# Optimization experiments

Measured on AMD Instinct MI355X. Metric: run time of the kernel, lower is better.

The kernel has to match this reference:

```python
import jax, jax.numpy as jnp
import numpy as np

DIMS = [3, 64, 64, 64, 3]  # [input_dim] + hidden dims + [input_dim]
TOTAL_W = sum(DIMS[l] * DIMS[l + 1] + 4 * DIMS[l + 1] for l in range(len(DIMS) - 1))  # 9356


def setup_inputs() -> dict:
    key = jax.random.key(0)
    k1, k2, k3 = jax.random.split(key, 3)
    B, N = 64, 8192
    context = jax.random.normal(k1, (B, N), dtype=jnp.float32)
    y = jax.random.normal(k2, (B, N, DIMS[0]), dtype=jnp.float32)
    tnw = jax.random.normal(k3, (B, TOTAL_W), dtype=jnp.float32) * 0.1
    return {"context": context, "y": y, "target_networks_weights": tnw}


def reference(context, y, target_networks_weights):
    B = target_networks_weights.shape[0]
    dx = y  # [B, N, dims[0]]
    i = 0
    n_layers = len(DIMS) - 1
    for l in range(n_layers):
        dl, dl1 = DIMS[l], DIMS[l + 1]
        W = target_networks_weights[:, i:i + dl * dl1].reshape(B, dl, dl1)
        i += dl * dl1
        bias = target_networks_weights[:, i:i + dl1]          # [B, dl1]
        i += dl1
        w_scale = target_networks_weights[:, i:i + dl1]        # [B, dl1]
        i += dl1
        b_scale = target_networks_weights[:, i:i + dl1]        # [B, dl1]
        i += dl1
        w_shift = target_networks_weights[:, i:i + dl1]        # [B, dl1]
        i += dl1
        # batched matmul + bias
        dx = jnp.einsum('bnd,bde->bne', dx, W) + bias[:, None, :]
        # sigmoid gate: bmm(context[:, :, None], w_scale[:, None, :]) = outer product
        scale = jax.nn.sigmoid(context[:, :, None] * w_scale[:, None, :] + b_scale[:, None, :])
        dx = scale * dx
        # shift term
        dx = dx + context[:, :, None] * w_shift[:, None, :]
        if l < n_layers - 1:
            dx = jax.nn.softplus(dx)
    return dx
```

## Files before the change

kernel.cpp:

```cpp
#include <hip/hip_runtime.h>
#include <math.h>

#define BB 64
#define NN 8192
#define TOTAL_W 9356

typedef _Float16 f16x8 __attribute__((ext_vector_type(8)));
typedef float f32x4 __attribute__((ext_vector_type(4)));
typedef float f32x2 __attribute__((ext_vector_type(2)));
typedef unsigned int u32x2 __attribute__((ext_vector_type(2)));

#define L2E 1.44269504088896340736f
#define LN2 0.6931471805599453f

#define FILM2_OFF 0
#define A1_OFF    4096
#define A2_OFF    (A1_OFF + 8192)
#define ACT_OFF   (A2_OFF + 8192)
#define LDS_BYTES (ACT_OFF + 128 * 128)

#define MFMA16(a, b, c) __builtin_amdgcn_mfma_f32_16x16x32_f16(a, b, c, 0, 0, 0)
#define EXP2 __builtin_amdgcn_exp2f
#define LOG2 __builtin_amdgcn_logf
#define RCPF __builtin_amdgcn_rcpf

__device__ __forceinline__ f32x2 pfma(f32x2 a, f32x2 b, f32x2 c) {
  return __builtin_elementwise_fma(a, b, c);
}

__device__ __forceinline__ const f32x4* film_base(const unsigned char* smem, int l, int qd) {
  return (const f32x4*)(smem + FILM2_OFF + ((l * 16 + qd) << 6));
}

template<bool SP>
__device__ __forceinline__ u32x2 film_quad(f32x4 acc, float ctx,
                                           f32x4 wscq, f32x4 bscq, f32x4 wshq) {
  f32x2 ctx2 = {ctx, ctx};
  f32x2 one = {1.f, 1.f};
  f32x2 z0 = pfma(ctx2, (f32x2){wscq.x, wscq.y}, (f32x2){bscq.x, bscq.y});
  f32x2 z1 = pfma(ctx2, (f32x2){wscq.z, wscq.w}, (f32x2){bscq.z, bscq.w});
  f32x2 d0 = {EXP2(-z0.x), EXP2(-z0.y)};  d0 += one;
  f32x2 d1 = {EXP2(-z1.x), EXP2(-z1.y)};  d1 += one;
  f32x2 s0 = {RCPF(d0.x), RCPF(d0.y)};
  f32x2 s1 = {RCPF(d1.x), RCPF(d1.y)};
  f32x2 v0 = pfma(ctx2, (f32x2){wshq.x, wshq.y}, s0 * (f32x2){acc.x, acc.y});
  f32x2 v1 = pfma(ctx2, (f32x2){wshq.z, wshq.w}, s1 * (f32x2){acc.z, acc.w});
  if (SP) {
    f32x2 l2 = {L2E, L2E}, ln = {LN2, LN2};
    f32x2 t0 = v0 * l2, t1 = v1 * l2;
    f32x2 u0 = {EXP2(t0.x), EXP2(t0.y)};  u0 += one;
    f32x2 u1 = {EXP2(t1.x), EXP2(t1.y)};  u1 += one;
    f32x2 g0 = {LOG2(u0.x), LOG2(u0.y)};
    f32x2 g1 = {LOG2(u1.x), LOG2(u1.y)};
    v0 = g0 * ln;
    v1 = g1 * ln;
  }
  auto p01 = __builtin_amdgcn_cvt_pkrtz(v0.x, v0.y);
  auto p23 = __builtin_amdgcn_cvt_pkrtz(v1.x, v1.y);
  u32x2 w;
  w.x = __builtin_bit_cast(unsigned int, p01);
  w.y = __builtin_bit_cast(unsigned int, p23);
  return w;
}

__device__ __forceinline__ void act_store(unsigned char* smem, int pt, int slot, u32x2 w) {
  int pos = ((((slot >> 1) ^ (pt & 7)) << 1) | (slot & 1));
  *(u32x2*)(smem + ACT_OFF + pt * 128 + (pos << 3)) = w;
}
__device__ __forceinline__ f16x8 act_load(const unsigned char* smem, int pt, int pair) {
  int gr = pair ^ (pt & 7);
  return *(const f16x8*)(smem + ACT_OFF + pt * 128 + (gr << 4));
}

__global__ __launch_bounds__(256)
void ode_hypernet_kernel(const float* __restrict__ context,
                         const float* __restrict__ y,
                         const float* __restrict__ tnw,
                         float* __restrict__ out) {
  __shared__ __align__(16) unsigned char smem[LDS_BYTES];
  const int b = blockIdx.y;
  const int tid = threadIdx.x;
  const float* __restrict__ wb = tnw + (size_t)b * TOTAL_W;

  const int lane = tid & 63;
  const int wid = tid >> 6;
  const int g = lane >> 4;
  const int col = lane & 15;

  if (tid < 64) {
    const int biaso[4] = {192, 4544, 8896, 9344};
    const int dim[4] = {64, 64, 64, 3};
#pragma unroll
    for (int l = 0; l < 4; ++l) {
      float bv = 0.f, wscv = 0.f, bscv = 0.f, wshv = 0.f;
      if (tid < dim[l]) {
        int bo = biaso[l], d = dim[l];
        bv = wb[bo + tid];
        wscv = wb[bo + d + tid] * L2E;
        bscv = wb[bo + 2 * d + tid] * L2E;
        wshv = wb[bo + 3 * d + tid];
      }
      float* f2 = (float*)(smem + FILM2_OFF + ((l * 16 + (tid >> 2)) << 6)) + (tid & 3);
      f2[0] = bv;
      f2[4] = wscv;
      f2[8] = bscv;
      f2[12] = wshv;
    }
  }
#pragma unroll
  for (int L = 0; L < 2; ++L) {
    const int woff = L ? 4800 : 448;
    const int aoff = L ? A2_OFF : A1_OFF;
#pragma unroll
    for (int it = 0; it < 4; ++it) {
      int idx = tid + it * 256;
      int f_in = idx >> 4;
      int q = idx & 15;
      f32x4 w4 = *(const f32x4*)(wb + woff + f_in * 64 + q * 4);
      int m = q >> 2;
      int c4 = (q & 3) * 4;
      int t = f_in >> 5;
      int h = (f_in >> 3) & 3;
      int i = f_in & 7;
      unsigned char* base = smem + aoff + (m * 128 + t * 64 + h * 16 + c4) * 16 + i * 2;
#pragma unroll
      for (int j = 0; j < 4; ++j)
        *(_Float16*)(base + j * 16) = (_Float16)w4[j];
    }
  }
  f16x8 A0r[4];
#pragma unroll
  for (int m = 0; m < 4; ++m) {
#pragma unroll
    for (int i = 0; i < 8; ++i)
      A0r[m][i] = (g == 0 && i < 3) ? (_Float16)wb[i * 64 + 16 * m + col] : (_Float16)0.f;
  }
  f16x8 A3r0, A3r1;
#pragma unroll
  for (int i = 0; i < 8; ++i) {
    A3r0[i] = (col < 3) ? (_Float16)wb[9152 + (8 * g + i) * 3 + col] : (_Float16)0.f;
    A3r1[i] = (col < 3) ? (_Float16)wb[9152 + (32 + 8 * g + i) * 3 + col] : (_Float16)0.f;
  }
  __syncthreads();

  const int pt0 = wid * 32 + col;
  const int pt1 = pt0 + 16;

  const int nb = blockIdx.x * 256;
  const size_t cb = (size_t)b * NN;
  float ctxs[4], yv[4][3];
#pragma unroll
  for (int k = 0; k < 4; ++k) {
    int n = nb + (k >> 1) * 128 + pt0 + (k & 1) * 16;
    ctxs[k] = context[cb + n];
    const float* yp = y + (cb + n) * 3;
    yv[k][0] = yp[0]; yv[k][1] = yp[1]; yv[k][2] = yp[2];
  }

#pragma unroll
  for (int ss = 0; ss < 2; ++ss) {
    const float ctx0 = ctxs[ss * 2], ctx1 = ctxs[ss * 2 + 1];
    const int n0 = nb + ss * 128 + pt0;
    const int n1 = n0 + 16;

    f16x8 By0 = {0, 0, 0, 0, 0, 0, 0, 0};
    f16x8 By1 = {0, 0, 0, 0, 0, 0, 0, 0};
    if (g == 0) {
      By0[0] = (_Float16)yv[ss * 2][0];
      By0[1] = (_Float16)yv[ss * 2][1];
      By0[2] = (_Float16)yv[ss * 2][2];
      By1[0] = (_Float16)yv[ss * 2 + 1][0];
      By1[1] = (_Float16)yv[ss * 2 + 1][1];
      By1[2] = (_Float16)yv[ss * 2 + 1][2];
    }

#pragma unroll
    for (int m = 0; m < 4; ++m) {
      const f32x4* fb = film_base(smem, 0, 4 * m + g);
      f32x4 biasq = fb[0], wscq = fb[1], bscq = fb[2], wshq = fb[3];
      f32x4 c0 = biasq, c1 = biasq;
      c0 = MFMA16(A0r[m], By0, c0);
      c1 = MFMA16(A0r[m], By1, c1);
      act_store(smem, pt0, 4 * m + g, film_quad<true>(c0, ctx0, wscq, bscq, wshq));
      act_store(smem, pt1, 4 * m + g, film_quad<true>(c1, ctx1, wscq, bscq, wshq));
    }

#pragma unroll
    for (int L = 1; L <= 2; ++L) {
      const int aoff = (L == 1) ? A1_OFF : A2_OFF;
      f16x8 B00 = act_load(smem, pt0, g);
      f16x8 B01 = act_load(smem, pt0, 4 + g);
      f16x8 B10 = act_load(smem, pt1, g);
      f16x8 B11 = act_load(smem, pt1, 4 + g);
#pragma unroll
      for (int m = 0; m < 4; ++m) {
        const f32x4* fb = film_base(smem, L, 4 * m + g);
        f32x4 biasq = fb[0], wscq = fb[1], bscq = fb[2], wshq = fb[3];
        f16x8 a0 = *(const f16x8*)(smem + aoff + ((m * 2 + 0) * 64 + lane) * 16);
        f16x8 a1 = *(const f16x8*)(smem + aoff + ((m * 2 + 1) * 64 + lane) * 16);
        f32x4 c0 = biasq, c1 = biasq;
        c0 = MFMA16(a0, B00, c0);
        c0 = MFMA16(a1, B01, c0);
        c1 = MFMA16(a0, B10, c1);
        c1 = MFMA16(a1, B11, c1);
        act_store(smem, pt0, 4 * m + g, film_quad<true>(c0, ctx0, wscq, bscq, wshq));
        act_store(smem, pt1, 4 * m + g, film_quad<true>(c1, ctx1, wscq, bscq, wshq));
      }
    }

    {
      f16x8 B00 = act_load(smem, pt0, g);
      f16x8 B01 = act_load(smem, pt0, 4 + g);
      f16x8 B10 = act_load(smem, pt1, g);
      f16x8 B11 = act_load(smem, pt1, 4 + g);
      const f32x4* fb = film_base(smem, 3, g);
      f32x4 biasq = fb[0], wscq = fb[1], bscq = fb[2], wshq = fb[3];
      f32x4 c0 = biasq, c1 = biasq;
      c0 = MFMA16(A3r0, B00, c0);
      c0 = MFMA16(A3r1, B01, c0);
      c1 = MFMA16(A3r0, B10, c1);
      c1 = MFMA16(A3r1, B11, c1);
      if (g == 0) {
#pragma unroll
        for (int p = 0; p < 2; ++p) {
          f32x4 c = p ? c1 : c0;
          float ctx = p ? ctx1 : ctx0;
          int n = p ? n1 : n0;
#pragma unroll
          for (int j = 0; j < 3; ++j) {
            float z = fmaf(ctx, wscq[j], bscq[j]);
            float s = RCPF(1.0f + EXP2(-z));
            float v = fmaf(ctx, wshq[j], s * c[j]);
            out[((size_t)b * NN + n) * 3 + j] = v;
          }
        }
      }
    }
  }
}

extern "C" void kernel_launch(void* const* d_in, const int* in_sizes, int n_in,
                              void* d_out, int out_size, void* d_ws, size_t ws_size,
                              hipStream_t stream) {
  const float* context = (const float*)d_in[0];
  const float* y       = (const float*)d_in[1];
  const float* tnw     = (const float*)d_in[2];
  float* out           = (float*)d_out;

  dim3 grid(NN / 256, BB, 1);
  dim3 block(256, 1, 1);
  ode_hypernet_kernel<<<grid, block, 0, stream>>>(context, y, tnw, out);
}
```

Before: 55.64 us.

## Precompute per-batch fp16 weight layouts in a prep kernel, copy into LDS

A new prep kernel runs once per batch. It converts the hypernetwork weights into the MFMA-ready fp16 layout plus FiLM parameters and writes them to a workspace buffer. The main kernel, which has 32 blocks per batch, then does a straight vectorized 16-byte copy of this preformatted data into LDS, replacing the scattered fp32 loads, conversions and strided stores each block did before. The cost is an extra kernel launch and a small serialization between the two kernels.

```diff
diff --git a/kernel.cpp b/kernel.cpp
--- a/kernel.cpp
+++ b/kernel.cpp
@@ -13,10 +13,17 @@
 #define L2E 1.44269504088896340736f
 #define LN2 0.6931471805599453f
 
+#define WS_FILM 0
+#define WS_A1   4096
+#define WS_A2   12288
+#define WS_A0   20480
+#define WS_A3   24576
+#define WSB     26624
+
 #define FILM2_OFF 0
 #define A1_OFF    4096
-#define A2_OFF    (A1_OFF + 8192)
-#define ACT_OFF   (A2_OFF + 8192)
+#define A2_OFF    12288
+#define ACT_OFF   20480
 #define LDS_BYTES (ACT_OFF + 128 * 128)
 
 #define MFMA16(a, b, c) __builtin_amdgcn_mfma_f32_16x16x32_f16(a, b, c, 0, 0, 0)
@@ -72,20 +79,12 @@
   return *(const f16x8*)(smem + ACT_OFF + pt * 128 + (gr << 4));
 }
 
-__global__ __launch_bounds__(256)
-void ode_hypernet_kernel(const float* __restrict__ context,
-                         const float* __restrict__ y,
-                         const float* __restrict__ tnw,
-                         float* __restrict__ out) {
-  __shared__ __align__(16) unsigned char smem[LDS_BYTES];
-  const int b = blockIdx.y;
+__global__ __launch_bounds__(512)
+void ode_prep_kernel(const float* __restrict__ tnw, unsigned char* __restrict__ ws) {
+  const int b = blockIdx.x;
   const int tid = threadIdx.x;
   const float* __restrict__ wb = tnw + (size_t)b * TOTAL_W;
-
-  const int lane = tid & 63;
-  const int wid = tid >> 6;
-  const int g = lane >> 4;
-  const int col = lane & 15;
+  unsigned char* __restrict__ wsb = ws + (size_t)b * WSB;
 
   if (tid < 64) {
     const int biaso[4] = {192, 4544, 8896, 9344};
@@ -100,7 +99,7 @@
         bscv = wb[bo + 2 * d + tid] * L2E;
         wshv = wb[bo + 3 * d + tid];
       }
-      float* f2 = (float*)(smem + FILM2_OFF + ((l * 16 + (tid >> 2)) << 6)) + (tid & 3);
+      float* f2 = (float*)(wsb + WS_FILM + ((l * 16 + (tid >> 2)) << 6)) + (tid & 3);
       f2[0] = bv;
       f2[4] = wscv;
       f2[8] = bscv;
@@ -110,37 +109,69 @@
 #pragma unroll
   for (int L = 0; L < 2; ++L) {
     const int woff = L ? 4800 : 448;
-    const int aoff = L ? A2_OFF : A1_OFF;
-#pragma unroll
-    for (int it = 0; it < 4; ++it) {
-      int idx = tid + it * 256;
-      int f_in = idx >> 4;
-      int q = idx & 15;
-      f32x4 w4 = *(const f32x4*)(wb + woff + f_in * 64 + q * 4);
-      int m = q >> 2;
-      int c4 = (q & 3) * 4;
-      int t = f_in >> 5;
-      int h = (f_in >> 3) & 3;
-      int i = f_in & 7;
-      unsigned char* base = smem + aoff + (m * 128 + t * 64 + h * 16 + c4) * 16 + i * 2;
-#pragma unroll
-      for (int j = 0; j < 4; ++j)
-        *(_Float16*)(base + j * 16) = (_Float16)w4[j];
-    }
+    unsigned char* dst = wsb + (L ? WS_A2 : WS_A1);
+    int r = tid;
+    int lane_r = r & 63;
+    int t = (r >> 6) & 1;
+    int m = r >> 7;
+    int f_out = 16 * m + (lane_r & 15);
+    int f_in0 = 32 * t + 8 * (lane_r >> 4);
+    f16x8 h;
+#pragma unroll
+    for (int i = 0; i < 8; ++i) h[i] = (_Float16)wb[woff + (f_in0 + i) * 64 + f_out];
+    *(f16x8*)(dst + r * 16) = h;
+  }
+  if (tid < 256) {
+    int m = tid >> 6;
+    int lane = tid & 63;
+    int g = lane >> 4, col = lane & 15;
+    f16x8 h = {0, 0, 0, 0, 0, 0, 0, 0};
+    if (g == 0) {
+#pragma unroll
+      for (int i = 0; i < 3; ++i) h[i] = (_Float16)wb[i * 64 + 16 * m + col];
+    }
+    *(f16x8*)(wsb + WS_A0 + tid * 16) = h;
+  }
+  if (tid < 128) {
+    int t = tid >> 6;
+    int lane = tid & 63;
+    int g = lane >> 4, col = lane & 15;
+    f16x8 h = {0, 0, 0, 0, 0, 0, 0, 0};
+    if (col < 3) {
+#pragma unroll
+      for (int i = 0; i < 8; ++i)
+        h[i] = (_Float16)wb[9152 + (32 * t + 8 * g + i) * 3 + col];
+    }
+    *(f16x8*)(wsb + WS_A3 + tid * 16) = h;
+  }
+}
+
+__global__ __launch_bounds__(256)
+void ode_hypernet_kernel(const float* __restrict__ context,
+                         const float* __restrict__ y,
+                         const unsigned char* __restrict__ ws,
+                         float* __restrict__ out) {
+  __shared__ __align__(16) unsigned char smem[LDS_BYTES];
+  const int b = blockIdx.y;
+  const int tid = threadIdx.x;
+  const unsigned char* __restrict__ wsb = ws + (size_t)b * WSB;
+
+  const int lane = tid & 63;
+  const int wid = tid >> 6;
+  const int g = lane >> 4;
+  const int col = lane & 15;
+
+#pragma unroll
+  for (int it = 0; it < 5; ++it) {
+    int i = tid + it * 256;
+    *(f32x4*)(smem + i * 16) = *(const f32x4*)(wsb + i * 16);
   }
   f16x8 A0r[4];
 #pragma unroll
-  for (int m = 0; m < 4; ++m) {
-#pragma unroll
-    for (int i = 0; i < 8; ++i)
-      A0r[m][i] = (g == 0 && i < 3) ? (_Float16)wb[i * 64 + 16 * m + col] : (_Float16)0.f;
-  }
-  f16x8 A3r0, A3r1;
-#pragma unroll
-  for (int i = 0; i < 8; ++i) {
-    A3r0[i] = (col < 3) ? (_Float16)wb[9152 + (8 * g + i) * 3 + col] : (_Float16)0.f;
-    A3r1[i] = (col < 3) ? (_Float16)wb[9152 + (32 + 8 * g + i) * 3 + col] : (_Float16)0.f;
-  }
+  for (int m = 0; m < 4; ++m)
+    A0r[m] = *(const f16x8*)(wsb + WS_A0 + (m * 64 + lane) * 16);
+  f16x8 A3r0 = *(const f16x8*)(wsb + WS_A3 + lane * 16);
+  f16x8 A3r1 = *(const f16x8*)(wsb + WS_A3 + (64 + lane) * 16);
   __syncthreads();
 
   const int pt0 = wid * 32 + col;
@@ -246,8 +277,10 @@
   const float* y       = (const float*)d_in[1];
   const float* tnw     = (const float*)d_in[2];
   float* out           = (float*)d_out;
-
+  unsigned char* ws    = (unsigned char*)d_ws;
+
+  ode_prep_kernel<<<dim3(BB, 1, 1), dim3(512, 1, 1), 0, stream>>>(tnw, ws);
   dim3 grid(NN / 256, BB, 1);
   dim3 block(256, 1, 1);
-  ode_hypernet_kernel<<<grid, block, 0, stream>>>(context, y, tnw, out);
-}
+  ode_hypernet_kernel<<<grid, block, 0, stream>>>(context, y, ws, out);
+}
```

After: 55.46 us. No clear change (-0.3%).
